# Optimization experiments

Hardware: AMD Instinct MI355X
Metric: run time of the kernel (lower is better)

Reference implementation:

```python
import jax, jax.numpy as jnp
import numpy as np

N_NODES = 50000
EMBED_DIM = 128
N_EDGES = 600000
ALPHA = 0.2  # LeakyReLU negative slope


def setup_inputs() -> dict:
    key = jax.random.key(0)
    k1, k2 = jax.random.split(key)
    drug_embeddings = jax.random.normal(k1, (N_NODES, EMBED_DIM), dtype=jnp.float32)
    drug_relationships = jax.random.randint(k2, (N_EDGES, 2), 0, N_NODES, dtype=jnp.int64)
    return {"drug_embeddings": drug_embeddings, "drug_relationships": drug_relationships}


def reference(drug_embeddings, drug_relationships):
    # edge_index = drug_relationships.T : row 0 = target/source node i, row 1 = neighbor j
    src = drug_relationships[:, 0]  # [E]
    dst = drug_relationships[:, 1]  # [E]
    drug_i = drug_embeddings[src]   # [E, D] gather
    drug_j = drug_embeddings[dst]   # [E, D] gather
    # per-edge dot-product score with LeakyReLU
    scores = jax.nn.leaky_relu(jnp.sum(drug_i * drug_j, axis=1), negative_slope=ALPHA)  # [E]
    # NOTE: original applies a single GLOBAL softmax over all edges (dim=0), not per-node
    att = jax.nn.softmax(scores, axis=0)  # [E]
    weighted = drug_j * att[:, None]      # [E, D]
    # scatter_add back onto source nodes
    h_prime = jax.ops.segment_sum(weighted, src, num_segments=drug_embeddings.shape[0])  # [N, D]
    return h_prime + drug_embeddings
```

## Files before the change

### kernel.cpp

```cpp
#include <hip/hip_runtime.h>
#include <math.h>

constexpr int kNodes = 50000;
constexpr int kEdges = 600000;
constexpr float kAlpha = 0.2f;
constexpr float kNegBig = -1e30f;

constexpr int kBlock = 256;
constexpr int kGrid  = 2048;
constexpr int kGStride = kGrid * kBlock;

constexpr int kGroups = 16;
constexpr int kBlocksPerGroup = kGrid / kGroups;

constexpr int kNodesPerBlock = 8;
constexpr int kNodeBlocks = kNodes / kNodesPerBlock;
constexpr int kMaxIt = (kNodeBlocks + kGrid - 1) / kGrid;

constexpr int kCap = 48;
constexpr int kWPN = kCap / 2;

constexpr int kOffFinal  = 8;
constexpr int kOffRoot   = 16;
constexpr int kOffGrp    = 32;
constexpr int kOffCounts = kOffGrp + kGroups * 32;
constexpr int kOffCsr    = kOffCounts + kNodes;
constexpr int kOffPart   = kOffCsr + kNodes * kWPN;
constexpr int kEndWs     = kOffPart + 2 * kGrid;

__device__ __forceinline__ void gridBarrier(int* wsi, int ord) {
    __syncthreads();
    if (threadIdx.x == 0) {
        asm volatile("s_waitcnt vmcnt(0) lgkmcnt(0)" ::: "memory");
        const int grp = blockIdx.x & (kGroups - 1);
        int* gc = wsi + kOffGrp + grp * 32;
        const int old = __hip_atomic_fetch_add(gc, 1, __ATOMIC_RELAXED, __HIP_MEMORY_SCOPE_AGENT);
        if (old == kBlocksPerGroup * ord - 1)
            __hip_atomic_fetch_add(wsi + kOffRoot, 1, __ATOMIC_RELAXED, __HIP_MEMORY_SCOPE_AGENT);
        while (__hip_atomic_load(wsi + kOffRoot, __ATOMIC_RELAXED, __HIP_MEMORY_SCOPE_AGENT)
               < kGroups * ord)
            __builtin_amdgcn_s_sleep(4);
    }
    __syncthreads();
}

__device__ __forceinline__ void onlineMerge(float& m, float& s, float m2, float s2) {
    const float M = fmaxf(m, m2);
    s = s * __expf(m - M) + s2 * __expf(m2 - M);
    m = M;
}

__global__ __launch_bounds__(kBlock, 8)
void fused_kernel(const float4* __restrict__ emb4,
                  const int2*  __restrict__ rel2,
                  float4*      __restrict__ out4,
                  float*       __restrict__ wsf)
{
    int* wsi = (int*)wsf;
    int*                counts = wsi + kOffCounts;
    unsigned int*       csr32  = (unsigned int*)(wsi + kOffCsr);
    const unsigned int* csr32c = (const unsigned int*)(wsi + kOffCsr);

    const int tid  = threadIdx.x;
    const int gtid = blockIdx.x * kBlock + tid;

    for (int e = gtid; e < kEdges; e += kGStride) {
        const int2 sd = rel2[e];
        const int pos = atomicAdd(&counts[sd.x], 1);
        if (pos < kCap)
            atomicOr(&csr32[sd.x * kWPN + (pos >> 1)],
                     (unsigned int)sd.y << ((pos & 1) * 16));
    }
    gridBarrier(wsi, 1);

    const int g    = tid & 31;
    const int grp8 = tid >> 5;
    const char* embB = (const char*)emb4;
    const unsigned g16 = (unsigned)g * 16u;

    float4 accv[kMaxIt];
    float  mrun[kMaxIt];
    float Mgrp = kNegBig, Sgrp = 0.0f;

    __shared__ float4 aLds[kMaxIt][kNodesPerBlock][32];

    #pragma unroll
    for (int it = 0; it < kMaxIt; ++it) {
        accv[it] = make_float4(0.f, 0.f, 0.f, 0.f);
        mrun[it] = kNegBig;
        const int vb = (int)blockIdx.x + it * kGrid;
        if (vb < kNodeBlocks) {
            const int node = vb * kNodesPerBlock + grp8;
            const float4 a = *(const float4*)(embB + ((unsigned)node * 512u + g16));
            aLds[it][grp8][g] = a;
            float4 acc = make_float4(0.f, 0.f, 0.f, 0.f);
            float m_run = kNegBig, s_run = 0.0f;

            const int cnt = min(counts[node], kCap);
            unsigned int lo = 0, hi = 0;
            if (g < kWPN && 2 * g < cnt) {
                const unsigned int w = csr32c[node * kWPN + g];
                lo = w & 0xffffu; hi = w >> 16;
            }

            int k = 0;
            for (; k + 3 < cnt; k += 4) {
                const int h = k >> 1;
                const int d0 = (int)__shfl(lo, h, 32);
                const int d1 = (int)__shfl(hi, h, 32);
                const int d2 = (int)__shfl(lo, h + 1, 32);
                const int d3 = (int)__shfl(hi, h + 1, 32);
                const float4 b0 = *(const float4*)(embB + ((unsigned)d0 * 512u + g16));
                const float4 b1 = *(const float4*)(embB + ((unsigned)d1 * 512u + g16));
                const float4 b2 = *(const float4*)(embB + ((unsigned)d2 * 512u + g16));
                const float4 b3 = *(const float4*)(embB + ((unsigned)d3 * 512u + g16));
                float p0 = a.x*b0.x + a.y*b0.y + a.z*b0.z + a.w*b0.w;
                float p1 = a.x*b1.x + a.y*b1.y + a.z*b1.z + a.w*b1.w;
                float p2 = a.x*b2.x + a.y*b2.y + a.z*b2.z + a.w*b2.w;
                float p3 = a.x*b3.x + a.y*b3.y + a.z*b3.z + a.w*b3.w;
                #pragma unroll
                for (int o = 16; o > 0; o >>= 1) {
                    p0 += __shfl_xor(p0, o); p1 += __shfl_xor(p1, o);
                    p2 += __shfl_xor(p2, o); p3 += __shfl_xor(p3, o);
                }
                const float s0 = p0 > 0.f ? p0 : kAlpha * p0;
                const float s1 = p1 > 0.f ? p1 : kAlpha * p1;
                const float s2 = p2 > 0.f ? p2 : kAlpha * p2;
                const float s3 = p3 > 0.f ? p3 : kAlpha * p3;
                const float m4 = fmaxf(fmaxf(s0, s1), fmaxf(s2, s3));
                if (m4 > m_run) {
                    const float rs = __expf(m_run - m4);
                    s_run *= rs;
                    acc.x *= rs; acc.y *= rs; acc.z *= rs; acc.w *= rs;
                    m_run = m4;
                }
                const float w0e = __expf(s0 - m_run);
                const float w1e = __expf(s1 - m_run);
                const float w2e = __expf(s2 - m_run);
                const float w3e = __expf(s3 - m_run);
                s_run += w0e + w1e + w2e + w3e;
                acc.x += w0e*b0.x + w1e*b1.x + w2e*b2.x + w3e*b3.x;
                acc.y += w0e*b0.y + w1e*b1.y + w2e*b2.y + w3e*b3.y;
                acc.z += w0e*b0.z + w1e*b1.z + w2e*b2.z + w3e*b3.z;
                acc.w += w0e*b0.w + w1e*b1.w + w2e*b2.w + w3e*b3.w;
            }
            for (; k < cnt; ++k) {
                const unsigned int wv = (k & 1) ? hi : lo;
                const int d0 = (int)__shfl(wv, k >> 1, 32);
                const float4 b0 = *(const float4*)(embB + ((unsigned)d0 * 512u + g16));
                float p0 = a.x*b0.x + a.y*b0.y + a.z*b0.z + a.w*b0.w;
                #pragma unroll
                for (int o = 16; o > 0; o >>= 1) p0 += __shfl_xor(p0, o);
                const float s0 = p0 > 0.f ? p0 : kAlpha * p0;
                if (s0 > m_run) {
                    const float rs = __expf(m_run - s0);
                    s_run *= rs;
                    acc.x *= rs; acc.y *= rs; acc.z *= rs; acc.w *= rs;
                    m_run = s0;
                }
                const float w0e = __expf(s0 - m_run);
                s_run += w0e;
                acc.x += w0e*b0.x; acc.y += w0e*b0.y; acc.z += w0e*b0.z; acc.w += w0e*b0.w;
            }

            accv[it] = acc;
            mrun[it] = m_run;
            onlineMerge(Mgrp, Sgrp, m_run, s_run);
        }
    }

    __shared__ float sm[kNodesPerBlock];
    __shared__ float ss[kNodesPerBlock];
    if (g == 0) { sm[grp8] = Mgrp; ss[grp8] = Sgrp; }
    __syncthreads();
    if (tid == 0) {
        float M = sm[0], S = ss[0];
        #pragma unroll
        for (int i = 1; i < kNodesPerBlock; ++i) onlineMerge(M, S, sm[i], ss[i]);
        float2 p = make_float2(M, S);
        unsigned long long bits;
        __builtin_memcpy(&bits, &p, 8);
        __hip_atomic_store((unsigned long long*)(wsi + kOffPart) + blockIdx.x, bits,
                           __ATOMIC_RELAXED, __HIP_MEMORY_SCOPE_AGENT);
    }
    gridBarrier(wsi, 2);

    if (blockIdx.x == 0) {
        float M = kNegBig, S = 0.0f;
        const float2* pp = (const float2*)(wsi + kOffPart);
        for (int i = tid; i < kGrid; i += kBlock) {
            const float2 p = pp[i];
            onlineMerge(M, S, p.x, p.y);
        }
        __shared__ float fm[kBlock];
        __shared__ float fs[kBlock];
        fm[tid] = M; fs[tid] = S;
        __syncthreads();
        for (int s = kBlock >> 1; s > 0; s >>= 1) {
            if (tid < s) {
                float m1 = fm[tid], s1 = fs[tid];
                onlineMerge(m1, s1, fm[tid + s], fs[tid + s]);
                fm[tid] = m1; fs[tid] = s1;
            }
            __syncthreads();
        }
        if (tid == 0) {
            float2 fin = make_float2(fm[0], 1.0f / fs[0]);
            unsigned long long bits;
            __builtin_memcpy(&bits, &fin, 8);
            __hip_atomic_store((unsigned long long*)(wsi + kOffFinal), bits,
                               __ATOMIC_RELAXED, __HIP_MEMORY_SCOPE_AGENT);
        }
    }
    gridBarrier(wsi, 3);

    {
        __shared__ float2 sfin;
        if (tid == 0) {
            const unsigned long long bits =
                __hip_atomic_load((const unsigned long long*)(wsi + kOffFinal),
                                  __ATOMIC_RELAXED, __HIP_MEMORY_SCOPE_AGENT);
            float2 f; __builtin_memcpy(&f, &bits, 8);
            sfin = f;
        }
        __syncthreads();
        const float gM    = sfin.x;
        const float gInvS = sfin.y;

        char* outB = (char*)out4;
        #pragma unroll
        for (int it = 0; it < kMaxIt; ++it) {
            const int vb = (int)blockIdx.x + it * kGrid;
            if (vb < kNodeBlocks) {
                const int node = vb * kNodesPerBlock + grp8;
                const float scale = __expf(mrun[it] - gM) * gInvS;
                const float4 e4 = aLds[it][grp8][g];
                const float4 o  = accv[it];
                *(float4*)(outB + ((unsigned)node * 512u + g16)) =
                    make_float4(e4.x + scale * o.x, e4.y + scale * o.y,
                                e4.z + scale * o.z, e4.w + scale * o.w);
            }
        }
    }
}

extern "C" void kernel_launch(void* const* d_in, const int* in_sizes, int n_in,
                              void* d_out, int out_size, void* d_ws, size_t ws_size,
                              hipStream_t stream) {
    const float4* emb4 = (const float4*)d_in[0];
    const int2*   rel2 = (const int2*)d_in[1];
    float4* out4 = (float4*)d_out;
    float*  wsf  = (float*)d_ws;
    int*    wsi  = (int*)d_ws;

    hipMemsetAsync(wsi + kOffRoot, 0,
                   (size_t)(kOffPart - kOffRoot) * sizeof(int), stream);
    hipLaunchKernelGGL(fused_kernel, dim3(kGrid), dim3(kBlock), 0, stream,
                       emb4, rel2, out4, wsf);
}
```

Before: 197.6 us.

## Gather neighbor embeddings as fp16 with one wave64 per node, drop final grid barrier

A pre-pass kernel writes an fp16 copy of the embedding table into the output buffer. The fused kernel then gathers neighbor rows from that copy, which halves the bytes moved by the dominant random-access traffic. Work is remapped so each 64-lane wave handles one node with two floats per lane, replacing 32-lane groups. The third grid barrier is replaced by blocks polling a non-zero final-softmax flag. The trade-offs are an extra conversion launch and reduced precision in the scores and weighted sums, which could exceed tolerance, since scores feed an exponential in a global softmax.

```diff
diff --git a/kernel.cpp b/kernel.cpp
--- a/kernel.cpp
+++ b/kernel.cpp
@@ -1,4 +1,5 @@
 #include <hip/hip_runtime.h>
+#include <hip/hip_fp16.h>
 #include <math.h>
 
 constexpr int kNodes = 50000;
@@ -13,9 +14,9 @@
 constexpr int kGroups = 16;
 constexpr int kBlocksPerGroup = kGrid / kGroups;
 
-constexpr int kNodesPerBlock = 8;
-constexpr int kNodeBlocks = kNodes / kNodesPerBlock;
-constexpr int kMaxIt = (kNodeBlocks + kGrid - 1) / kGrid;
+constexpr int kWaves = 4;
+constexpr int kTasks = kNodes / kWaves;
+constexpr int kSlots = (kTasks + kGrid - 1) / kGrid;
 
 constexpr int kCap = 48;
 constexpr int kWPN = kCap / 2;
@@ -27,6 +28,8 @@
 constexpr int kOffCsr    = kOffCounts + kNodes;
 constexpr int kOffPart   = kOffCsr + kNodes * kWPN;
 constexpr int kEndWs     = kOffPart + 2 * kGrid;
+
+struct __align__(8) H4 { __half2 lo, hi; };
 
 __device__ __forceinline__ void gridBarrier(int* wsi, int ord) {
     __syncthreads();
@@ -50,6 +53,17 @@
     m = M;
 }
 
+__global__ void conv_kernel(const float4* __restrict__ emb4, H4* __restrict__ embh) {
+    for (int i = blockIdx.x * blockDim.x + threadIdx.x; i < kNodes * 32;
+         i += gridDim.x * blockDim.x) {
+        const float4 v = emb4[i];
+        H4 r;
+        r.lo = __floats2half2_rn(v.x, v.y);
+        r.hi = __floats2half2_rn(v.z, v.w);
+        embh[i] = r;
+    }
+}
+
 __global__ __launch_bounds__(kBlock, 8)
 void fused_kernel(const float4* __restrict__ emb4,
                   const int2*  __restrict__ rel2,
@@ -73,55 +87,52 @@
     }
     gridBarrier(wsi, 1);
 
-    const int g    = tid & 31;
-    const int grp8 = tid >> 5;
-    const char* embB = (const char*)emb4;
-    const unsigned g16 = (unsigned)g * 16u;
-
-    float4 accv[kMaxIt];
-    float  mrun[kMaxIt];
-    float Mgrp = kNegBig, Sgrp = 0.0f;
-
-    __shared__ float4 aLds[kMaxIt][kNodesPerBlock][32];
+    const int lane = tid & 63;
+    const int wave = tid >> 6;
+    const float2*  emb2  = (const float2*)emb4;
+    const __half2* embh2 = (const __half2*)out4;
+
+    float2 accv[kSlots];
+    float  mrun[kSlots];
+    float Mw = kNegBig, Sw = 0.0f;
 
     #pragma unroll
-    for (int it = 0; it < kMaxIt; ++it) {
-        accv[it] = make_float4(0.f, 0.f, 0.f, 0.f);
+    for (int it = 0; it < kSlots; ++it) {
+        accv[it] = make_float2(0.f, 0.f);
         mrun[it] = kNegBig;
-        const int vb = (int)blockIdx.x + it * kGrid;
-        if (vb < kNodeBlocks) {
-            const int node = vb * kNodesPerBlock + grp8;
-            const float4 a = *(const float4*)(embB + ((unsigned)node * 512u + g16));
-            aLds[it][grp8][g] = a;
-            float4 acc = make_float4(0.f, 0.f, 0.f, 0.f);
+        const int t = (int)blockIdx.x + it * kGrid;
+        if (t < kTasks) {
+            const int node = t * kWaves + wave;
+            const float2 a = emb2[(unsigned)node * 64u + lane];
+            float2 acc = make_float2(0.f, 0.f);
             float m_run = kNegBig, s_run = 0.0f;
 
             const int cnt = min(counts[node], kCap);
             unsigned int lo = 0, hi = 0;
-            if (g < kWPN && 2 * g < cnt) {
-                const unsigned int w = csr32c[node * kWPN + g];
+            if (lane < kWPN && 2 * lane < cnt) {
+                const unsigned int w = csr32c[node * kWPN + lane];
                 lo = w & 0xffffu; hi = w >> 16;
             }
 
             int k = 0;
             for (; k + 3 < cnt; k += 4) {
                 const int h = k >> 1;
-                const int d0 = (int)__shfl(lo, h, 32);
-                const int d1 = (int)__shfl(hi, h, 32);
-                const int d2 = (int)__shfl(lo, h + 1, 32);
-                const int d3 = (int)__shfl(hi, h + 1, 32);
-                const float4 b0 = *(const float4*)(embB + ((unsigned)d0 * 512u + g16));
-                const float4 b1 = *(const float4*)(embB + ((unsigned)d1 * 512u + g16));
-                const float4 b2 = *(const float4*)(embB + ((unsigned)d2 * 512u + g16));
-                const float4 b3 = *(const float4*)(embB + ((unsigned)d3 * 512u + g16));
-                float p0 = a.x*b0.x + a.y*b0.y + a.z*b0.z + a.w*b0.w;
-                float p1 = a.x*b1.x + a.y*b1.y + a.z*b1.z + a.w*b1.w;
-                float p2 = a.x*b2.x + a.y*b2.y + a.z*b2.z + a.w*b2.w;
-                float p3 = a.x*b3.x + a.y*b3.y + a.z*b3.z + a.w*b3.w;
+                const int d0 = (int)__shfl(lo, h, 64);
+                const int d1 = (int)__shfl(hi, h, 64);
+                const int d2 = (int)__shfl(lo, h + 1, 64);
+                const int d3 = (int)__shfl(hi, h + 1, 64);
+                const float2 b0 = __half22float2(embh2[(unsigned)d0 * 64u + lane]);
+                const float2 b1 = __half22float2(embh2[(unsigned)d1 * 64u + lane]);
+                const float2 b2 = __half22float2(embh2[(unsigned)d2 * 64u + lane]);
+                const float2 b3 = __half22float2(embh2[(unsigned)d3 * 64u + lane]);
+                float p0 = a.x*b0.x + a.y*b0.y;
+                float p1 = a.x*b1.x + a.y*b1.y;
+                float p2 = a.x*b2.x + a.y*b2.y;
+                float p3 = a.x*b3.x + a.y*b3.y;
                 #pragma unroll
-                for (int o = 16; o > 0; o >>= 1) {
-                    p0 += __shfl_xor(p0, o); p1 += __shfl_xor(p1, o);
-                    p2 += __shfl_xor(p2, o); p3 += __shfl_xor(p3, o);
+                for (int o = 32; o > 0; o >>= 1) {
+                    p0 += __shfl_xor(p0, o, 64); p1 += __shfl_xor(p1, o, 64);
+                    p2 += __shfl_xor(p2, o, 64); p3 += __shfl_xor(p3, o, 64);
                 }
                 const float s0 = p0 > 0.f ? p0 : kAlpha * p0;
                 const float s1 = p1 > 0.f ? p1 : kAlpha * p1;
@@ -131,7 +142,7 @@
                 if (m4 > m_run) {
                     const float rs = __expf(m_run - m4);
                     s_run *= rs;
-                    acc.x *= rs; acc.y *= rs; acc.z *= rs; acc.w *= rs;
+                    acc.x *= rs; acc.y *= rs;
                     m_run = m4;
                 }
                 const float w0e = __expf(s0 - m_run);
@@ -141,42 +152,40 @@
                 s_run += w0e + w1e + w2e + w3e;
                 acc.x += w0e*b0.x + w1e*b1.x + w2e*b2.x + w3e*b3.x;
                 acc.y += w0e*b0.y + w1e*b1.y + w2e*b2.y + w3e*b3.y;
-                acc.z += w0e*b0.z + w1e*b1.z + w2e*b2.z + w3e*b3.z;
-                acc.w += w0e*b0.w + w1e*b1.w + w2e*b2.w + w3e*b3.w;
             }
             for (; k < cnt; ++k) {
                 const unsigned int wv = (k & 1) ? hi : lo;
-                const int d0 = (int)__shfl(wv, k >> 1, 32);
-                const float4 b0 = *(const float4*)(embB + ((unsigned)d0 * 512u + g16));
-                float p0 = a.x*b0.x + a.y*b0.y + a.z*b0.z + a.w*b0.w;
+                const int d0 = (int)__shfl(wv, k >> 1, 64);
+                const float2 b0 = __half22float2(embh2[(unsigned)d0 * 64u + lane]);
+                float p0 = a.x*b0.x + a.y*b0.y;
                 #pragma unroll
-                for (int o = 16; o > 0; o >>= 1) p0 += __shfl_xor(p0, o);
+                for (int o = 32; o > 0; o >>= 1) p0 += __shfl_xor(p0, o, 64);
                 const float s0 = p0 > 0.f ? p0 : kAlpha * p0;
                 if (s0 > m_run) {
                     const float rs = __expf(m_run - s0);
                     s_run *= rs;
-                    acc.x *= rs; acc.y *= rs; acc.z *= rs; acc.w *= rs;
+                    acc.x *= rs; acc.y *= rs;
                     m_run = s0;
                 }
                 const float w0e = __expf(s0 - m_run);
                 s_run += w0e;
-                acc.x += w0e*b0.x; acc.y += w0e*b0.y; acc.z += w0e*b0.z; acc.w += w0e*b0.w;
+                acc.x += w0e*b0.x; acc.y += w0e*b0.y;
             }
 
             accv[it] = acc;
             mrun[it] = m_run;
-            onlineMerge(Mgrp, Sgrp, m_run, s_run);
-        }
-    }
-
-    __shared__ float sm[kNodesPerBlock];
-    __shared__ float ss[kNodesPerBlock];
-    if (g == 0) { sm[grp8] = Mgrp; ss[grp8] = Sgrp; }
+            onlineMerge(Mw, Sw, m_run, s_run);
+        }
+    }
+
+    __shared__ float sm[kWaves];
+    __shared__ float ss[kWaves];
+    if (lane == 0) { sm[wave] = Mw; ss[wave] = Sw; }
     __syncthreads();
     if (tid == 0) {
         float M = sm[0], S = ss[0];
         #pragma unroll
-        for (int i = 1; i < kNodesPerBlock; ++i) onlineMerge(M, S, sm[i], ss[i]);
+        for (int i = 1; i < kWaves; ++i) onlineMerge(M, S, sm[i], ss[i]);
         float2 p = make_float2(M, S);
         unsigned long long bits;
         __builtin_memcpy(&bits, &p, 8);
@@ -212,14 +221,17 @@
                                __ATOMIC_RELAXED, __HIP_MEMORY_SCOPE_AGENT);
         }
     }
-    gridBarrier(wsi, 3);
 
     {
         __shared__ float2 sfin;
         if (tid == 0) {
-            const unsigned long long bits =
-                __hip_atomic_load((const unsigned long long*)(wsi + kOffFinal),
-                                  __ATOMIC_RELAXED, __HIP_MEMORY_SCOPE_AGENT);
+            unsigned long long bits;
+            for (;;) {
+                bits = __hip_atomic_load((const unsigned long long*)(wsi + kOffFinal),
+                                         __ATOMIC_RELAXED, __HIP_MEMORY_SCOPE_AGENT);
+                if (bits != 0ull) break;
+                __builtin_amdgcn_s_sleep(2);
+            }
             float2 f; __builtin_memcpy(&f, &bits, 8);
             sfin = f;
         }
@@ -227,18 +239,17 @@
         const float gM    = sfin.x;
         const float gInvS = sfin.y;
 
-        char* outB = (char*)out4;
+        float2* out2 = (float2*)out4;
         #pragma unroll
-        for (int it = 0; it < kMaxIt; ++it) {
-            const int vb = (int)blockIdx.x + it * kGrid;
-            if (vb < kNodeBlocks) {
-                const int node = vb * kNodesPerBlock + grp8;
+        for (int it = 0; it < kSlots; ++it) {
+            const int t = (int)blockIdx.x + it * kGrid;
+            if (t < kTasks) {
+                const int node = t * kWaves + wave;
                 const float scale = __expf(mrun[it] - gM) * gInvS;
-                const float4 e4 = aLds[it][grp8][g];
-                const float4 o  = accv[it];
-                *(float4*)(outB + ((unsigned)node * 512u + g16)) =
-                    make_float4(e4.x + scale * o.x, e4.y + scale * o.y,
-                                e4.z + scale * o.z, e4.w + scale * o.w);
+                const float2 e = emb2[(unsigned)node * 64u + lane];
+                const float2 o = accv[it];
+                out2[(unsigned)node * 64u + lane] =
+                    make_float2(e.x + scale * o.x, e.y + scale * o.y);
             }
         }
     }
@@ -253,8 +264,10 @@
     float*  wsf  = (float*)d_ws;
     int*    wsi  = (int*)d_ws;
 
-    hipMemsetAsync(wsi + kOffRoot, 0,
-                   (size_t)(kOffPart - kOffRoot) * sizeof(int), stream);
+    hipMemsetAsync(wsi + kOffFinal, 0,
+                   (size_t)(kOffPart - kOffFinal) * sizeof(int), stream);
+    hipLaunchKernelGGL(conv_kernel, dim3(1024), dim3(kBlock), 0, stream,
+                       emb4, (H4*)d_out);
     hipLaunchKernelGGL(fused_kernel, dim3(kGrid), dim3(kBlock), 0, stream,
                        emb4, rel2, out4, wsf);
 }
```

New measurement: 205.1 us. +3.8%, slower.
